# Performance work log

Measured on AMD Instinct MI355X. Metric: run time of the kernel, lower is better.

Reference implementation:

```python
import jax, jax.numpy as jnp
import numpy as np

POOL_H, POOL_W = 7, 7
N_ROI = 300
H, W, C = 200, 200, 512


def setup_inputs() -> dict:
    key = jax.random.key(0)
    k1, k2, k3 = jax.random.split(key, 3)
    image = jax.random.normal(k1, (1, H, W, C), dtype=jnp.float32)
    xy = jax.random.randint(k2, (1, N_ROI, 2), 0, 160)   # x, y
    wh = jax.random.randint(k3, (1, N_ROI, 2), 1, 40)    # w, h >= 1
    rois = jnp.concatenate([xy, wh], axis=-1).astype(jnp.float32)  # (1, N_ROI, 4)
    return {"image": image, "rois": rois}


def _roi_pool_one(fmap, roi):
    # fmap: (H, W, C); roi: (4,) = (x, y, w, h), cast to int as in the original.
    x = roi[0].astype(jnp.int32)
    y = roi[1].astype(jnp.int32)
    w = roi[2].astype(jnp.int32)
    h = roi[3].astype(jnp.int32)
    # Legacy tf.image.resize_images bilinear (align_corners=False, no half-pixel
    # centers): src_coord = out_coord * (in_size / out_size), lerp between
    # floor and min(floor+1, in_size-1).
    sy = jnp.arange(POOL_H, dtype=jnp.float32) * (h.astype(jnp.float32) / POOL_H)
    sx = jnp.arange(POOL_W, dtype=jnp.float32) * (w.astype(jnp.float32) / POOL_W)
    y0 = jnp.floor(sy).astype(jnp.int32)
    y1 = jnp.minimum(y0 + 1, h - 1)
    fy = sy - y0.astype(jnp.float32)
    x0 = jnp.floor(sx).astype(jnp.int32)
    x1 = jnp.minimum(x0 + 1, w - 1)
    fx = sx - x0.astype(jnp.float32)
    # Separable bilinear: interpolate rows, then columns.
    rows = (fmap[y + y0] * (1.0 - fy)[:, None, None]
            + fmap[y + y1] * fy[:, None, None])               # (POOL_H, W, C)
    out = (rows[:, x + x0] * (1.0 - fx)[None, :, None]
           + rows[:, x + x1] * fx[None, :, None])             # (POOL_H, POOL_W, C)
    return out


def reference(image, rois):
    # image: (1, H, W, C); rois: (1, N_ROI, 4). Original only reads batch 0.
    pooled = jax.vmap(lambda r: _roi_pool_one(image[0], r))(rois[0])
    return pooled[None]  # (1, N_ROI, POOL_H, POOL_W, C)
```

## Files before the change

kernel.cpp:

```cpp
#include <hip/hip_runtime.h>


#define POOL   7
#define N_ROI  300
#define IMG_W  200
#define CH4    128
#define NCELL  (N_ROI * POOL * POOL)
#define NBLK   (NCELL / 2)
#define NXCD   8

typedef float f4 __attribute__((ext_vector_type(4)));

struct Cell {
    int c00, c01, c10, c11;
    float w00, w01, w10, w11;
};

__device__ inline Cell decode_cell(const f4* __restrict__ rois4, int b) {
    const int q = b % POOL;
    const int t = b / POOL;
    const int p = t % POOL;
    const int r = t / POOL;

    const f4 rv = rois4[r];
    const int x = (int)rv.x;
    const int y = (int)rv.y;
    const int w = (int)rv.z;
    const int h = (int)rv.w;

    const float sy = (float)p * ((float)h / 7.0f);
    const int y0 = (int)floorf(sy);
    const int y1 = min(y0 + 1, h - 1);
    const float fy = sy - (float)y0;

    const float sx = (float)q * ((float)w / 7.0f);
    const int x0 = (int)floorf(sx);
    const int x1 = min(x0 + 1, w - 1);
    const float fx = sx - (float)x0;

    const int row0 = (y + y0) * IMG_W;
    const int row1 = (y + y1) * IMG_W;

    Cell cl;
    cl.c00 = (row0 + x + x0) * CH4;
    cl.c01 = (row0 + x + x1) * CH4;
    cl.c10 = (row1 + x + x0) * CH4;
    cl.c11 = (row1 + x + x1) * CH4;
    cl.w00 = (1.0f - fy) * (1.0f - fx);
    cl.w01 = (1.0f - fy) * fx;
    cl.w10 = fy * (1.0f - fx);
    cl.w11 = fy * fx;
    return cl;
}

__device__ inline f4 blend(f4 a, f4 b, f4 c, f4 d,
                           float wa, float wb, float wc, float wd) {
    return a * wa + b * wb + c * wc + d * wd;
}

__global__ __launch_bounds__(CH4) void roi_pool_kernel(
        const float* __restrict__ image,
        const float* __restrict__ rois,
        float* __restrict__ out) {
    const int bid = blockIdx.x;
    const int qc = NBLK / NXCD;
    const int rm = NBLK % NXCD;
    const int xcd = bid % NXCD;
    const int idx = bid / NXCD;
    const int blk = (xcd < rm ? xcd * (qc + 1)
                              : rm * (qc + 1) + (xcd - rm) * qc) + idx;

    const int c = threadIdx.x;
    const f4* __restrict__ img4  = (const f4*)image;
    const f4* __restrict__ rois4 = (const f4*)rois;
    f4* __restrict__ out4 = (f4*)out;

    const int b0 = blk * 2;
    const int b1 = b0 + 1;

    const Cell cA = decode_cell(rois4, b0);
    const Cell cB = decode_cell(rois4, b1);

    const f4 a00 = img4[cA.c00 + c];
    const f4 a01 = img4[cA.c01 + c];
    const f4 a10 = img4[cA.c10 + c];
    const f4 a11 = img4[cA.c11 + c];
    const f4 b00 = img4[cB.c00 + c];
    const f4 b01 = img4[cB.c01 + c];
    const f4 b10 = img4[cB.c10 + c];
    const f4 b11 = img4[cB.c11 + c];

    const f4 oA = blend(a00, a01, a10, a11, cA.w00, cA.w01, cA.w10, cA.w11);
    const f4 oB = blend(b00, b01, b10, b11, cB.w00, cB.w01, cB.w10, cB.w11);

    __builtin_nontemporal_store(oA, &out4[b0 * CH4 + c]);
    __builtin_nontemporal_store(oB, &out4[b1 * CH4 + c]);
}

extern "C" void kernel_launch(void* const* d_in, const int* in_sizes, int n_in,
                              void* d_out, int out_size, void* d_ws, size_t ws_size,
                              hipStream_t stream) {
    const float* image = (const float*)d_in[0];
    const float* rois  = (const float*)d_in[1];
    float* out = (float*)d_out;

    roi_pool_kernel<<<NBLK, CH4, 0, stream>>>(image, rois, out);
}
```

Before: 21.85 us.

## Sort ROIs by Morton-ordered center to improve cache locality across XCDs

Adds a single-block bitonic sort kernel that orders ROIs by the Morton code of their centers and writes a permutation into workspace. The pooling kernel then walks ROIs in sorted order, so spatially nearby ROIs land on the same XCD and can share L2 lines for image reads, and it scatters outputs back to their original positions. The cost is an extra kernel launch plus a serial dependency on the sort.

Result: slower. 25.58 us (+17.1%).

```diff
diff --git a/kernel.cpp b/kernel.cpp
--- a/kernel.cpp
+++ b/kernel.cpp
@@ -8,19 +8,56 @@
 #define NCELL  (N_ROI * POOL * POOL)
 #define NBLK   (NCELL / 2)
 #define NXCD   8
+#define SORTN  512
 
 typedef float f4 __attribute__((ext_vector_type(4)));
 
+__global__ __launch_bounds__(SORTN) void sort_rois_kernel(
+        const float* __restrict__ rois,
+        unsigned* __restrict__ perm) {
+    __shared__ unsigned key[SORTN];
+    const int t = threadIdx.x;
+    unsigned k = 0xFFFFFFFFu;
+    if (t < N_ROI) {
+        const f4 rv = ((const f4*)rois)[t];
+        const int cx = (int)rv.x + ((int)rv.z >> 1);
+        const int cy = (int)rv.y + ((int)rv.w >> 1);
+        unsigned m = 0;
+        #pragma unroll
+        for (int i = 0; i < 8; ++i)
+            m |= (((unsigned)(cx >> i) & 1u) << (2 * i))
+               | (((unsigned)(cy >> i) & 1u) << (2 * i + 1));
+        k = (m << 9) | (unsigned)t;
+    }
+    key[t] = k;
+    __syncthreads();
+    for (int sz = 2; sz <= SORTN; sz <<= 1) {
+        for (int st = sz >> 1; st > 0; st >>= 1) {
+            const int j = t ^ st;
+            if (j > t) {
+                const unsigned a = key[t], b = key[j];
+                const bool up = ((t & sz) == 0);
+                if ((a > b) == up) { key[t] = b; key[j] = a; }
+            }
+            __syncthreads();
+        }
+    }
+    if (t < N_ROI) perm[t] = key[t] & 0x1FFu;
+}
+
 struct Cell {
     int c00, c01, c10, c11;
+    int outc;
     float w00, w01, w10, w11;
 };
 
-__device__ inline Cell decode_cell(const f4* __restrict__ rois4, int b) {
-    const int q = b % POOL;
-    const int t = b / POOL;
-    const int p = t % POOL;
-    const int r = t / POOL;
+__device__ inline Cell decode_cell(const f4* __restrict__ rois4,
+                                   const unsigned* __restrict__ perm, int b) {
+    const int q  = b % POOL;
+    const int tt = b / POOL;
+    const int p  = tt % POOL;
+    const int rs = tt / POOL;
+    const int r  = perm ? (int)perm[rs] : rs;
 
     const f4 rv = rois4[r];
     const int x = (int)rv.x;
@@ -46,6 +83,7 @@
     cl.c01 = (row0 + x + x1) * CH4;
     cl.c10 = (row1 + x + x0) * CH4;
     cl.c11 = (row1 + x + x1) * CH4;
+    cl.outc = (r * (POOL * POOL) + (b - rs * (POOL * POOL))) * CH4;
     cl.w00 = (1.0f - fy) * (1.0f - fx);
     cl.w01 = (1.0f - fy) * fx;
     cl.w10 = fy * (1.0f - fx);
@@ -61,6 +99,7 @@
 __global__ __launch_bounds__(CH4) void roi_pool_kernel(
         const float* __restrict__ image,
         const float* __restrict__ rois,
+        const unsigned* __restrict__ perm,
         float* __restrict__ out) {
     const int bid = blockIdx.x;
     const int qc = NBLK / NXCD;
@@ -78,8 +117,8 @@
     const int b0 = blk * 2;
     const int b1 = b0 + 1;
 
-    const Cell cA = decode_cell(rois4, b0);
-    const Cell cB = decode_cell(rois4, b1);
+    const Cell cA = decode_cell(rois4, perm, b0);
+    const Cell cB = decode_cell(rois4, perm, b1);
 
     const f4 a00 = img4[cA.c00 + c];
     const f4 a01 = img4[cA.c01 + c];
@@ -93,8 +132,8 @@
     const f4 oA = blend(a00, a01, a10, a11, cA.w00, cA.w01, cA.w10, cA.w11);
     const f4 oB = blend(b00, b01, b10, b11, cB.w00, cB.w01, cB.w10, cB.w11);
 
-    __builtin_nontemporal_store(oA, &out4[b0 * CH4 + c]);
-    __builtin_nontemporal_store(oB, &out4[b1 * CH4 + c]);
+    __builtin_nontemporal_store(oA, &out4[cA.outc + c]);
+    __builtin_nontemporal_store(oB, &out4[cB.outc + c]);
 }
 
 extern "C" void kernel_launch(void* const* d_in, const int* in_sizes, int n_in,
@@ -104,5 +143,11 @@
     const float* rois  = (const float*)d_in[1];
     float* out = (float*)d_out;
 
-    roi_pool_kernel<<<NBLK, CH4, 0, stream>>>(image, rois, out);
+    if (ws_size >= N_ROI * sizeof(unsigned)) {
+        unsigned* perm = (unsigned*)d_ws;
+        sort_rois_kernel<<<1, SORTN, 0, stream>>>(rois, perm);
+        roi_pool_kernel<<<NBLK, CH4, 0, stream>>>(image, rois, perm, out);
+    } else {
+        roi_pool_kernel<<<NBLK, CH4, 0, stream>>>(image, rois, nullptr, out);
+    }
 }
```
